# Kernel tuning notes

Measured on AMD Instinct MI355X. Metric: run time of the kernel, lower is better.

## Reference

```python
import jax, jax.numpy as jnp
import numpy as np

TOP_K = 2000
NUM_DETS = 1000
BASE_LAYER_RANGE = (24.0, 48.0, 24.0, 48.0)  # (min_y, max_y, min_x, max_x) from db.configs


def _topk(heat, K):
    # heat: [B, C, H, W] -> topk over flattened C*H*W (CornerNet-style)
    B, C, H, W = heat.shape
    scores, inds = jax.lax.top_k(heat.reshape(B, -1), K)
    clses = inds // (H * W)
    sp_inds = inds % (H * W)            # spatial index into H*W
    ys = (sp_inds // W).astype(heat.dtype)
    xs = (sp_inds % W).astype(heat.dtype)
    return scores, sp_inds, clses, ys, xs


def _transpose_and_gather(feat, ind):
    # feat: [B, C, H, W], ind: [B, K] spatial indices -> [B, K, C]
    B, C, H, W = feat.shape
    feat = feat.transpose(0, 2, 3, 1).reshape(B, H * W, C)
    return feat[jnp.arange(B)[:, None], ind]


def _gather_feat(feat, ind):
    # feat: [B, N, C], ind: [B, K] -> [B, K, C]
    B = feat.shape[0]
    return feat[jnp.arange(B)[:, None], ind]


def _decode_layer(heat, tl_regr, br_regr, H0, W0, layer_idx):
    B, C, H, W = heat.shape
    dt = heat.dtype
    height_scale = 8.0 * H0 / H
    width_scale = 8.0 * W0 / W
    K = min(TOP_K, H * W)
    scores, inds, clses, ys, xs = _topk(heat, K)
    ys = ys.reshape(B, K, 1)
    xs = xs.reshape(B, K, 1)
    tlr = _transpose_and_gather(tl_regr, inds).reshape(B, K, 1, 2)
    brr = _transpose_and_gather(br_regr, inds).reshape(B, K, 1, 2)
    min_y, max_y, min_x, max_x = [v / 8.0 / 2.0 for v in BASE_LAYER_RANGE]
    tl_xs = xs - ((max_x - min_x) * tlr[..., 0] + (max_x + min_x) / 2.0)
    tl_ys = ys - ((max_y - min_y) * tlr[..., 1] + (max_y + min_y) / 2.0)
    br_xs = xs + ((max_x - min_x) * brr[..., 0] + (max_x + min_x) / 2.0)
    br_ys = ys + ((max_y - min_y) * brr[..., 1] + (max_y + min_y) / 2.0)
    bboxes = jnp.stack((tl_xs, tl_ys, br_xs, br_ys), axis=3)  # [B, K, 1, 4]
    sc = scores.reshape(B, K, 1)
    invalid = (br_xs < tl_xs) | (br_ys < tl_ys)
    sc = jnp.where(invalid, jnp.asarray(-1.0, dt), sc)
    sc = sc.reshape(B, -1)
    nd = min(NUM_DETS, sc.shape[1])
    sc, top = jax.lax.top_k(sc, nd)
    sc = sc[:, :, None]
    bboxes = _gather_feat(bboxes.reshape(B, -1, 4), top)
    bboxes = bboxes * jnp.asarray([width_scale, height_scale, width_scale, height_scale], dt)
    # layer_detections: zeros [B, nd, 7]; [:,:,:5] = cat([scores, bboxes]); then row 6 set to i
    det = jnp.concatenate([sc, bboxes, jnp.zeros((B, nd, 2), dt)], axis=2)
    det = det.at[:, 6, :].set(jnp.asarray(float(layer_idx), dt))  # faithful to `[:, 6] = i`
    return det


def setup_inputs() -> dict:
    key = jax.random.key(0)
    ks = jax.random.split(key, 9)
    B, C = 16, 80
    sizes = [(128, 128), (64, 64), (32, 32)]
    inp = {}
    for i, (H, W) in enumerate(sizes):
        inp[f"heat{i}"] = jax.random.uniform(ks[3 * i], (B, C, H, W), dtype=jnp.float32)
        inp[f"tl{i}"] = jax.random.normal(ks[3 * i + 1], (B, 2, H, W), dtype=jnp.float32)
        inp[f"br{i}"] = jax.random.normal(ks[3 * i + 2], (B, 2, H, W), dtype=jnp.float32)
    return inp


def reference(heat0, heat1, heat2, tl0, tl1, tl2, br0, br1, br2):
    heats = [heat0, heat1, heat2]
    tls = [tl0, tl1, tl2]
    brs = [br0, br1, br2]
    _, _, H0, W0 = heats[0].shape
    dets = [_decode_layer(heats[i], tls[i], brs[i], H0, W0, i) for i in range(3)]
    detections = jnp.concatenate(dets, axis=1)  # [B, sum_nd, 7]
    nd = min(NUM_DETS, detections.shape[1])
    _, top = jax.lax.top_k(detections[:, :, 0], nd)
    return _gather_feat(detections, top)
```

## Files before the change

kernel.cpp:

```cpp
#include <hip/hip_runtime.h>


#define NB 1024
#define CAP2 2048
#define CHUNK 32768

__device__ __forceinline__ unsigned int ord_f32(float f) {
    unsigned int b = __float_as_uint(f);
    return (b & 0x80000000u) ? ~b : (b | 0x80000000u);
}
__device__ __forceinline__ float unord_f32(unsigned int o) {
    unsigned int b = (o & 0x80000000u) ? (o & 0x7fffffffu) : ~o;
    return __uint_as_float(b);
}
__device__ __forceinline__ int bucket_of(float f) {
    int bi = (int)(f * (float)NB);
    bi = bi < 0 ? 0 : (bi > NB - 1 ? NB - 1 : bi);
    return bi;
}

__device__ __forceinline__ int layer_N(int l)  { return (l == 0) ? 1310720 : (l == 1) ? 327680 : 81920; }
__device__ __forceinline__ int nchunks(int l)  { return (l == 0) ? 40 : (l == 1) ? 10 : 3; }
__device__ __forceinline__ int hist_base(int l){ return (l == 0) ? 0 : (l == 1) ? 640 : 800; }
__device__ __forceinline__ int TL_of(int l)    { return (l == 0) ? NB - 4 : (l == 1) ? NB - 16 : NB - 32; }
__device__ __forceinline__ int bl_cap(int l)   { return (l == 0) ? 512 : (l == 1) ? 1024 : 2048; }
__device__ __forceinline__ int loose_base(int l){ return (l == 0) ? 0 : (l == 1) ? 327680 : 491520; }

__global__ __launch_bounds__(256) void fused_kernel(
    const float* __restrict__ h0, const float* __restrict__ h1, const float* __restrict__ h2,
    int* __restrict__ ph, int* __restrict__ pbc, unsigned long long* __restrict__ loose)
{
    int l = blockIdx.z, b = blockIdx.y, chunk = blockIdx.x;
    int nc = nchunks(l);
    if (chunk >= nc) return;
    int N = layer_N(l);
    int elems = min(CHUNK, N - chunk * CHUNK);
    const float* heat = (l == 0) ? h0 : (l == 1) ? h1 : h2;
    int TL = TL_of(l);

    __shared__ int lh[NB];
    __shared__ int lc;
    __shared__ unsigned long long lbuf[2048];
    for (int i = threadIdx.x; i < NB; i += 256) lh[i] = 0;
    if (threadIdx.x == 0) lc = 0;
    __syncthreads();

    const float4* p = (const float4*)(heat + (size_t)b * N + (size_t)chunk * CHUNK);
    int base = chunk * CHUNK;
    int n4 = elems >> 2;
    for (int i = threadIdx.x; i < n4; i += 256) {
        float4 v = p[i];
        float vs[4] = {v.x, v.y, v.z, v.w};
#pragma unroll
        for (int cc = 0; cc < 4; cc++) {
            int bk = bucket_of(vs[cc]);
            atomicAdd(&lh[bk], 1);
            if (bk >= TL) {
                int pos = atomicAdd(&lc, 1);
                if (pos < 2048) {
                    unsigned int idx = (unsigned int)(base + 4 * i + cc);
                    lbuf[pos] = ((unsigned long long)ord_f32(vs[cc]) << 32) | (unsigned int)(~idx);
                }
            }
        }
    }
    __syncthreads();
    int pidx = hist_base(l) + b * nc + chunk;
    int* dst = ph + (size_t)pidx * NB;
    for (int i = threadIdx.x; i < NB; i += 256) dst[i] = lh[i];
    if (threadIdx.x == 0) pbc[pidx] = lc;
    int cap = bl_cap(l);
    int n = min(lc, min(cap, 2048));
    unsigned long long* seg = loose + loose_base(l) + (size_t)(b * nc + chunk) * cap;
    for (int i = threadIdx.x; i < n; i += 256) seg[i] = lbuf[i];
}

__global__ __launch_bounds__(256) void partition_kernel(
    const float* __restrict__ h0, const float* __restrict__ h1, const float* __restrict__ h2,
    const int* __restrict__ ph, const int* __restrict__ pbc,
    const unsigned long long* __restrict__ loose,
    int* __restrict__ cnt, unsigned long long* __restrict__ cand)
{
    int b = blockIdx.x & 15;
    int l = blockIdx.x >> 4;
    int bl = l * 16 + b;
    int K = (l == 2) ? 1024 : 2000;
    int nc = nchunks(l);
    int cap = bl_cap(l);
    const int* hbase = ph + (size_t)(hist_base(l) + b * nc) * NB;

    __shared__ int hh[NB];
    __shared__ int seg[256];
    __shared__ int st;
    __shared__ int repf;
    __shared__ int lc[2];
    __shared__ unsigned long long lbuf[2][2048];
    int tid = threadIdx.x;

    int s4 = 0;
    for (int j = 0; j < 4; j++) {
        int bkt = tid * 4 + j;
        int s = 0;
        for (int c = 0; c < nc; c++) s += hbase[(size_t)c * NB + bkt];
        hh[bkt] = s;
        s4 += s;
    }
    seg[tid] = s4;
    if (tid == 0) { repf = 0; lc[0] = 0; lc[1] = 0; }
    __syncthreads();
    if (tid == 0) {
        int acc = 0, si;
        for (si = 255; si >= 0; si--) {
            if (acc + seg[si] >= K) break;
            acc += seg[si];
        }
        if (si < 0) si = 0;
        int bidx = si * 4 + 3;
        for (; bidx > si * 4; bidx--) {
            acc += hh[bidx];
            if (acc >= K) break;
        }
        st = bidx;
        if (bidx < TL_of(l)) repf = 1;
    }
    __syncthreads();
    int t = st;
    for (int c = tid; c < nc; c += 256)
        if (pbc[hist_base(l) + b * nc + c] > min(cap, 2048)) repf = 1;
    __syncthreads();

    if (!repf) {
        const unsigned long long* lb = loose + loose_base(l) + (size_t)b * nc * cap;
        for (int c = 0; c < nc; c++) {
            int n_c = min(pbc[hist_base(l) + b * nc + c], min(cap, 2048));
            const unsigned long long* sg = lb + (size_t)c * cap;
            for (int i = tid; i < n_c; i += 256) {
                unsigned long long key = sg[i];
                int bk = bucket_of(unord_f32((unsigned int)(key >> 32)));
                if (bk >= t) {
                    int which = (bk > t) ? 0 : 1;
                    int pos = atomicAdd(&lc[which], 1);
                    if (pos < 2048) lbuf[which][pos] = key;
                }
            }
        }
    } else {
        int N = layer_N(l);
        const float* heat = (l == 0) ? h0 : (l == 1) ? h1 : h2;
        const float4* p = (const float4*)(heat + (size_t)b * N);
        for (int i = tid; i < (N >> 2); i += 256) {
            float4 v = p[i];
            float vs[4] = {v.x, v.y, v.z, v.w};
#pragma unroll
            for (int cc = 0; cc < 4; cc++) {
                int bk = bucket_of(vs[cc]);
                if (bk >= t) {
                    int which = (bk > t) ? 0 : 1;
                    int pos = atomicAdd(&lc[which], 1);
                    if (pos < 2048) {
                        unsigned int idx = (unsigned int)(4 * i + cc);
                        lbuf[which][pos] = ((unsigned long long)ord_f32(vs[cc]) << 32) | (unsigned int)(~idx);
                    }
                }
            }
        }
    }
    __syncthreads();
#pragma unroll
    for (int w = 0; w < 2; w++) {
        int n = min(lc[w], CAP2);
        if (tid == 0) cnt[bl * 2 + w] = n;
        unsigned long long* cd = cand + ((size_t)bl * 2 + w) * CAP2;
        for (int i = tid; i < n; i += 256) cd[i] = lbuf[w][i];
    }
}


__device__ __forceinline__ unsigned long long shfl_xor_u64(unsigned long long a, int j) {
    unsigned int lo = (unsigned int)a, hi = (unsigned int)(a >> 32);
    lo = (unsigned int)__shfl_xor((int)lo, j, 64);
    hi = (unsigned int)__shfl_xor((int)hi, j, 64);
    return ((unsigned long long)hi << 32) | lo;
}

template<int K, int J>
struct PhaseH {
    static __device__ __forceinline__ void run(unsigned long long (&v)[8], int base, int lane) {
        constexpr int JR = J >> 6;
#pragma unroll
        for (int r = 0; r < 8; r++) {
            if ((r & JR) == 0) {
                int i = base | (r << 6) | lane;
                unsigned long long a = v[r], bb = v[r | JR];
                bool sw = ((i & K) == 0) ? (a < bb) : (a > bb);
                if (sw) { v[r] = bb; v[r | JR] = a; }
            }
        }
        PhaseH<K, (J >> 1)>::run(v, base, lane);
    }
};

template<int K>
struct PhaseH<K, 32> {
    static __device__ __forceinline__ void run(unsigned long long (&v)[8], int base, int lane) {
#pragma unroll
        for (int js = 32; js >= 1; js >>= 1) {
            if (K > js) {
#pragma unroll
                for (int r = 0; r < 8; r++) {
                    unsigned long long a = v[r];
                    unsigned long long w = shfl_xor_u64(a, js);
                    int i = base | (r << 6) | lane;
                    bool upper = (lane & js) != 0;
                    bool keep_max = (((i & K) == 0) != upper);
                    bool agw = a > w;
                    v[r] = (keep_max == agw) ? a : w;
                }
            }
        }
    }
};

template<int K>
struct StageH {
    static __device__ __forceinline__ void run(unsigned long long (&v)[8], int base, int lane) {
        PhaseH<K, (K > 64 ? (K >> 1) : 32)>::run(v, base, lane);
        StageH<(K << 1)>::run(v, base, lane);
    }
};
template<>
struct StageH<1024> {
    static __device__ __forceinline__ void run(unsigned long long (&)[8], int, int) {}
};

template<int K, int J>
__device__ __forceinline__ void lds_exchange(unsigned long long (&v)[8],
                                             unsigned long long* lds, int base, int lane) {
    __syncthreads();
#pragma unroll
    for (int r = 0; r < 8; r++) lds[base | (r << 6) | lane] = v[r];
    __syncthreads();
#pragma unroll
    for (int r = 0; r < 8; r++) {
        int i = base | (r << 6) | lane;
        unsigned long long w = lds[i ^ J];
        bool upper = (i & J) != 0;
        bool keep_max = (((i & K) == 0) != upper);
        bool agw = v[r] > w;
        v[r] = (keep_max == agw) ? v[r] : w;
    }
}

__global__ __launch_bounds__(256) void sort_kernel(const int* __restrict__ cnt,
                                                   unsigned long long* __restrict__ cand)
{
    int idx = blockIdx.x;
    int n = min(cnt[idx], CAP2);
    unsigned long long* src = cand + (size_t)idx * CAP2;
    __shared__ unsigned long long lds[CAP2];
    int tid = threadIdx.x;
    int lane = tid & 63;
    int base = (tid >> 6) << 9;

    unsigned long long v[8];
#pragma unroll
    for (int r = 0; r < 8; r++) {
        int i = base | (r << 6) | lane;
        v[r] = (i < n) ? src[i] : 0ull;
    }

    StageH<2>::run(v, base, lane);

    lds_exchange<1024, 512>(v, lds, base, lane);
    PhaseH<1024, 256>::run(v, base, lane);

    lds_exchange<2048, 1024>(v, lds, base, lane);
    lds_exchange<2048, 512>(v, lds, base, lane);
    PhaseH<2048, 256>::run(v, base, lane);

#pragma unroll
    for (int r = 0; r < 8; r++) src[base | (r << 6) | lane] = v[r];
}

__global__ __launch_bounds__(1024) void build_kernel(
    const float* __restrict__ t0, const float* __restrict__ t1, const float* __restrict__ t2,
    const float* __restrict__ r0, const float* __restrict__ r1, const float* __restrict__ r2,
    const int* __restrict__ cnt, const unsigned long long* __restrict__ cand,
    float* __restrict__ det)
{
    int l = blockIdx.x >> 4;
    int b = blockIdx.x & 15;
    int bl = l * 16 + b;
    int HW = (l == 0) ? 16384 : (l == 1) ? 4096 : 1024;
    int W  = (l == 0) ? 128 : (l == 1) ? 64 : 32;
    int K  = (l == 2) ? 1024 : 2000;
    float scale = (l == 0) ? 8.f : (l == 1) ? 16.f : 32.f;
    const float* tlp = (l == 0) ? t0 : (l == 1) ? t1 : t2;
    const float* brp = (l == 0) ? r0 : (l == 1) ? r1 : r2;

    int n_hi = min(cnt[bl * 2], CAP2);
    const unsigned long long* hi = cand + (size_t)(bl * 2) * CAP2;
    const unsigned long long* bd = cand + (size_t)(bl * 2 + 1) * CAP2;

    __shared__ int wsum[16];
    int tid = threadIdx.x;
    int lane = tid & 63, wid = tid >> 6;

    float s_[2], bx_[2][4];
    int f_[2];
#pragma unroll
    for (int q = 0; q < 2; q++) {
        int k = 2 * tid + q;
        f_[q] = 0;
        if (k < K) {
            unsigned long long kk = (k < n_hi) ? hi[k] : bd[k - n_hi];
            unsigned int idx = ~(unsigned int)kk;
            float score = unord_f32((unsigned int)(kk >> 32));
            int sp = (int)(idx % (unsigned)HW);
            float xs = (float)(sp % W), ys = (float)(sp / W);
            float tv0 = tlp[((size_t)b * 2 + 0) * HW + sp];
            float tv1 = tlp[((size_t)b * 2 + 1) * HW + sp];
            float bv0 = brp[((size_t)b * 2 + 0) * HW + sp];
            float bv1 = brp[((size_t)b * 2 + 1) * HW + sp];
            float tlx = __fsub_rn(xs, __fadd_rn(__fmul_rn(1.5f, tv0), 2.25f));
            float tly = __fsub_rn(ys, __fadd_rn(__fmul_rn(1.5f, tv1), 2.25f));
            float brx = __fadd_rn(xs, __fadd_rn(__fmul_rn(1.5f, bv0), 2.25f));
            float bry = __fadd_rn(ys, __fadd_rn(__fmul_rn(1.5f, bv1), 2.25f));
            bool invalid = (brx < tlx) || (bry < tly);
            f_[q] = invalid ? 0 : 1;
            s_[q] = invalid ? -1.0f : score;
            bx_[q][0] = __fmul_rn(tlx, scale);
            bx_[q][1] = __fmul_rn(tly, scale);
            bx_[q][2] = __fmul_rn(brx, scale);
            bx_[q][3] = __fmul_rn(bry, scale);
        }
    }
    int mysum = f_[0] + f_[1];

    int x = mysum;
#pragma unroll
    for (int off = 1; off < 64; off <<= 1) {
        int y = __shfl_up(x, off, 64);
        if (lane >= off) x += y;
    }
    if (lane == 63) wsum[wid] = x;
    __syncthreads();
    if (wid == 0 && lane < 16) {
        int s = wsum[lane];
#pragma unroll
        for (int off = 1; off < 16; off <<= 1) {
            int y = __shfl_up(s, off, 64);
            if (lane >= off) s += y;
        }
        wsum[lane] = s;
    }
    __syncthreads();
    int wave_off = (wid > 0) ? wsum[wid - 1] : 0;
    int V = wsum[15];
    int base_excl = (x + wave_off) - mysum;

    float* dbase = det + ((size_t)b * 3000 + (size_t)l * 1000) * 7;
#pragma unroll
    for (int q = 0; q < 2; q++) {
        int k = 2 * tid + q;
        if (k < K) {
            int pos = base_excl + (q == 1 ? f_[0] : 0);
            int rank = f_[q] ? pos : V + (k - pos);
            if (rank < 1000 && rank != 6) {
                float* drow = dbase + (size_t)rank * 7;
                drow[0] = s_[q];
                drow[1] = bx_[q][0];
                drow[2] = bx_[q][1];
                drow[3] = bx_[q][2];
                drow[4] = bx_[q][3];
                drow[5] = 0.f;
                drow[6] = 0.f;
            }
        }
    }
    if (tid == 0) {
        float lv = (float)l;
        float* drow = dbase + 6 * 7;
#pragma unroll
        for (int j = 0; j < 7; j++) drow[j] = lv;
    }
}

__device__ __forceinline__ bool key_gt(float sa, int ga, float sb, int gb) {
    return (sa > sb) || (sa == sb && ga < gb);
}

__global__ __launch_bounds__(1024) void final_kernel(const float* __restrict__ det,
                                                     float* __restrict__ out)
{
    int b = blockIdx.x;
    __shared__ float sc[3000];
    int tid = threadIdx.x;
    const float* dbase = det + (size_t)b * 3000 * 7;
    for (int i = tid; i < 3000; i += 1024) sc[i] = dbase[(size_t)i * 7];
    __syncthreads();

    for (int e = tid; e < 3000; e += 1024) {
        float se = sc[e];
        int ge = e;
        int rank = 0;
#pragma unroll
        for (int lp = 0; lp < 3; lp++) {
            int lo = 0, hiB = 999;
            while (lo < hiB) {
                int mid = (lo + hiB) >> 1;
                int p = mid + (mid >= 6 ? 1 : 0);
                int g = lp * 1000 + p;
                if (key_gt(sc[g], g, se, ge)) lo = mid + 1; else hiB = mid;
            }
            rank += lo;
        }
#pragma unroll
        for (int ls = 0; ls < 3; ls++) {
            int g = ls * 1000 + 6;
            if (g != e && key_gt((float)ls, g, se, ge)) rank++;
        }
        if (rank < 1000) {
            const float* src = dbase + (size_t)e * 7;
            float* dst = out + ((size_t)b * 1000 + rank) * 7;
#pragma unroll
            for (int j = 0; j < 7; j++) dst[j] = src[j];
        }
    }
}

extern "C" void kernel_launch(void* const* d_in, const int* in_sizes, int n_in,
                              void* d_out, int out_size, void* d_ws, size_t ws_size,
                              hipStream_t stream)
{
    (void)in_sizes; (void)n_in; (void)out_size; (void)ws_size;
    const float* h0 = (const float*)d_in[0];
    const float* t0 = (const float*)d_in[1];
    const float* r0 = (const float*)d_in[2];
    const float* h1 = (const float*)d_in[3];
    const float* t1 = (const float*)d_in[4];
    const float* r1 = (const float*)d_in[5];
    const float* h2 = (const float*)d_in[6];
    const float* t2 = (const float*)d_in[7];
    const float* r2 = (const float*)d_in[8];
    float* out = (float*)d_out;

    char* ws = (char*)d_ws;
    int* ph   = (int*)ws;
    int* pbc  = (int*)(ws + 3473408);
    unsigned long long* loose = (unsigned long long*)(ws + 3476800);
    int* cnt  = (int*)(ws + 8195392);
    unsigned long long* cand  = (unsigned long long*)(ws + 8195776);
    float* det = (float*)(ws + 9768640);

    fused_kernel<<<dim3(40, 16, 3), 256, 0, stream>>>(h0, h1, h2, ph, pbc, loose);
    partition_kernel<<<48, 256, 0, stream>>>(h0, h1, h2, ph, pbc, loose, cnt, cand);
    sort_kernel<<<96, 256, 0, stream>>>(cnt, cand);
    build_kernel<<<48, 1024, 0, stream>>>(t0, t1, t2, r0, r1, r2, cnt, cand, det);
    final_kernel<<<16, 1024, 0, stream>>>(det, out);
}
```

Baseline: 255.7 us.

## Drop histogram pass; collect over fixed threshold and sort all candidates directly

The collect kernel no longer builds a per-chunk 1024-bucket histogram with shared atomics. It only gathers elements above a fixed per-layer threshold into smaller per-chunk segments. The separate partition kernel is removed, and the sort kernel concatenates the segments into a 4096-entry bitonic sort per batch-layer, holding 16 values per thread. That removes one launch, the histogram atomics and their global writes. In exchange the sort is larger, and a slow fallback (full-layer histogram plus rescan by one block) runs if too few or too many candidates are collected.

```diff
diff --git a/kernel.cpp b/kernel.cpp
--- a/kernel.cpp
+++ b/kernel.cpp
@@ -2,7 +2,6 @@
 
 
 #define NB 1024
-#define CAP2 2048
 #define CHUNK 32768
 
 __device__ __forceinline__ unsigned int ord_f32(float f) {
@@ -19,16 +18,16 @@
     return bi;
 }
 
-__device__ __forceinline__ int layer_N(int l)  { return (l == 0) ? 1310720 : (l == 1) ? 327680 : 81920; }
-__device__ __forceinline__ int nchunks(int l)  { return (l == 0) ? 40 : (l == 1) ? 10 : 3; }
-__device__ __forceinline__ int hist_base(int l){ return (l == 0) ? 0 : (l == 1) ? 640 : 800; }
-__device__ __forceinline__ int TL_of(int l)    { return (l == 0) ? NB - 4 : (l == 1) ? NB - 16 : NB - 32; }
-__device__ __forceinline__ int bl_cap(int l)   { return (l == 0) ? 512 : (l == 1) ? 1024 : 2048; }
-__device__ __forceinline__ int loose_base(int l){ return (l == 0) ? 0 : (l == 1) ? 327680 : 491520; }
-
-__global__ __launch_bounds__(256) void fused_kernel(
+__device__ __forceinline__ int layer_N(int l)   { return (l == 0) ? 1310720 : (l == 1) ? 327680 : 81920; }
+__device__ __forceinline__ int nchunks(int l)   { return (l == 0) ? 40 : (l == 1) ? 10 : 3; }
+__device__ __forceinline__ int chunk_base(int l){ return (l == 0) ? 0 : (l == 1) ? 640 : 800; }
+__device__ __forceinline__ float TL_of(int l)   { return (l == 0) ? 0.998046875f : (l == 1) ? 0.9921875f : 0.98125f; }
+__device__ __forceinline__ int seg_cap(int l)   { return (l == 0) ? 256 : (l == 1) ? 768 : 1024; }
+__device__ __forceinline__ int loose_base(int l){ return (l == 0) ? 0 : (l == 1) ? 163840 : 286720; }
+
+__global__ __launch_bounds__(256) void collect_kernel(
     const float* __restrict__ h0, const float* __restrict__ h1, const float* __restrict__ h2,
-    int* __restrict__ ph, int* __restrict__ pbc, unsigned long long* __restrict__ loose)
+    int* __restrict__ pbc, unsigned long long* __restrict__ loose)
 {
     int l = blockIdx.z, b = blockIdx.y, chunk = blockIdx.x;
     int nc = nchunks(l);
@@ -36,12 +35,10 @@
     int N = layer_N(l);
     int elems = min(CHUNK, N - chunk * CHUNK);
     const float* heat = (l == 0) ? h0 : (l == 1) ? h1 : h2;
-    int TL = TL_of(l);
-
-    __shared__ int lh[NB];
+    float TL = TL_of(l);
+
     __shared__ int lc;
-    __shared__ unsigned long long lbuf[2048];
-    for (int i = threadIdx.x; i < NB; i += 256) lh[i] = 0;
+    __shared__ unsigned long long lbuf[1024];
     if (threadIdx.x == 0) lc = 0;
     __syncthreads();
 
@@ -53,11 +50,9 @@
         float vs[4] = {v.x, v.y, v.z, v.w};
 #pragma unroll
         for (int cc = 0; cc < 4; cc++) {
-            int bk = bucket_of(vs[cc]);
-            atomicAdd(&lh[bk], 1);
-            if (bk >= TL) {
+            if (vs[cc] >= TL) {
                 int pos = atomicAdd(&lc, 1);
-                if (pos < 2048) {
+                if (pos < 1024) {
                     unsigned int idx = (unsigned int)(base + 4 * i + cc);
                     lbuf[pos] = ((unsigned long long)ord_f32(vs[cc]) << 32) | (unsigned int)(~idx);
                 }
@@ -65,114 +60,12 @@
         }
     }
     __syncthreads();
-    int pidx = hist_base(l) + b * nc + chunk;
-    int* dst = ph + (size_t)pidx * NB;
-    for (int i = threadIdx.x; i < NB; i += 256) dst[i] = lh[i];
+    int pidx = chunk_base(l) + b * nc + chunk;
     if (threadIdx.x == 0) pbc[pidx] = lc;
-    int cap = bl_cap(l);
-    int n = min(lc, min(cap, 2048));
+    int cap = seg_cap(l);
+    int n = min(lc, cap);
     unsigned long long* seg = loose + loose_base(l) + (size_t)(b * nc + chunk) * cap;
     for (int i = threadIdx.x; i < n; i += 256) seg[i] = lbuf[i];
-}
-
-__global__ __launch_bounds__(256) void partition_kernel(
-    const float* __restrict__ h0, const float* __restrict__ h1, const float* __restrict__ h2,
-    const int* __restrict__ ph, const int* __restrict__ pbc,
-    const unsigned long long* __restrict__ loose,
-    int* __restrict__ cnt, unsigned long long* __restrict__ cand)
-{
-    int b = blockIdx.x & 15;
-    int l = blockIdx.x >> 4;
-    int bl = l * 16 + b;
-    int K = (l == 2) ? 1024 : 2000;
-    int nc = nchunks(l);
-    int cap = bl_cap(l);
-    const int* hbase = ph + (size_t)(hist_base(l) + b * nc) * NB;
-
-    __shared__ int hh[NB];
-    __shared__ int seg[256];
-    __shared__ int st;
-    __shared__ int repf;
-    __shared__ int lc[2];
-    __shared__ unsigned long long lbuf[2][2048];
-    int tid = threadIdx.x;
-
-    int s4 = 0;
-    for (int j = 0; j < 4; j++) {
-        int bkt = tid * 4 + j;
-        int s = 0;
-        for (int c = 0; c < nc; c++) s += hbase[(size_t)c * NB + bkt];
-        hh[bkt] = s;
-        s4 += s;
-    }
-    seg[tid] = s4;
-    if (tid == 0) { repf = 0; lc[0] = 0; lc[1] = 0; }
-    __syncthreads();
-    if (tid == 0) {
-        int acc = 0, si;
-        for (si = 255; si >= 0; si--) {
-            if (acc + seg[si] >= K) break;
-            acc += seg[si];
-        }
-        if (si < 0) si = 0;
-        int bidx = si * 4 + 3;
-        for (; bidx > si * 4; bidx--) {
-            acc += hh[bidx];
-            if (acc >= K) break;
-        }
-        st = bidx;
-        if (bidx < TL_of(l)) repf = 1;
-    }
-    __syncthreads();
-    int t = st;
-    for (int c = tid; c < nc; c += 256)
-        if (pbc[hist_base(l) + b * nc + c] > min(cap, 2048)) repf = 1;
-    __syncthreads();
-
-    if (!repf) {
-        const unsigned long long* lb = loose + loose_base(l) + (size_t)b * nc * cap;
-        for (int c = 0; c < nc; c++) {
-            int n_c = min(pbc[hist_base(l) + b * nc + c], min(cap, 2048));
-            const unsigned long long* sg = lb + (size_t)c * cap;
-            for (int i = tid; i < n_c; i += 256) {
-                unsigned long long key = sg[i];
-                int bk = bucket_of(unord_f32((unsigned int)(key >> 32)));
-                if (bk >= t) {
-                    int which = (bk > t) ? 0 : 1;
-                    int pos = atomicAdd(&lc[which], 1);
-                    if (pos < 2048) lbuf[which][pos] = key;
-                }
-            }
-        }
-    } else {
-        int N = layer_N(l);
-        const float* heat = (l == 0) ? h0 : (l == 1) ? h1 : h2;
-        const float4* p = (const float4*)(heat + (size_t)b * N);
-        for (int i = tid; i < (N >> 2); i += 256) {
-            float4 v = p[i];
-            float vs[4] = {v.x, v.y, v.z, v.w};
-#pragma unroll
-            for (int cc = 0; cc < 4; cc++) {
-                int bk = bucket_of(vs[cc]);
-                if (bk >= t) {
-                    int which = (bk > t) ? 0 : 1;
-                    int pos = atomicAdd(&lc[which], 1);
-                    if (pos < 2048) {
-                        unsigned int idx = (unsigned int)(4 * i + cc);
-                        lbuf[which][pos] = ((unsigned long long)ord_f32(vs[cc]) << 32) | (unsigned int)(~idx);
-                    }
-                }
-            }
-        }
-    }
-    __syncthreads();
-#pragma unroll
-    for (int w = 0; w < 2; w++) {
-        int n = min(lc[w], CAP2);
-        if (tid == 0) cnt[bl * 2 + w] = n;
-        unsigned long long* cd = cand + ((size_t)bl * 2 + w) * CAP2;
-        for (int i = tid; i < n; i += 256) cd[i] = lbuf[w][i];
-    }
 }
 
 
@@ -184,11 +77,11 @@
 }
 
 template<int K, int J>
-struct PhaseH {
-    static __device__ __forceinline__ void run(unsigned long long (&v)[8], int base, int lane) {
+struct P16 {
+    static __device__ __forceinline__ void run(unsigned long long (&v)[16], int base, int lane) {
         constexpr int JR = J >> 6;
 #pragma unroll
-        for (int r = 0; r < 8; r++) {
+        for (int r = 0; r < 16; r++) {
             if ((r & JR) == 0) {
                 int i = base | (r << 6) | lane;
                 unsigned long long a = v[r], bb = v[r | JR];
@@ -196,18 +89,18 @@
                 if (sw) { v[r] = bb; v[r | JR] = a; }
             }
         }
-        PhaseH<K, (J >> 1)>::run(v, base, lane);
+        P16<K, (J >> 1)>::run(v, base, lane);
     }
 };
 
 template<int K>
-struct PhaseH<K, 32> {
-    static __device__ __forceinline__ void run(unsigned long long (&v)[8], int base, int lane) {
+struct P16<K, 32> {
+    static __device__ __forceinline__ void run(unsigned long long (&v)[16], int base, int lane) {
 #pragma unroll
         for (int js = 32; js >= 1; js >>= 1) {
             if (K > js) {
 #pragma unroll
-                for (int r = 0; r < 8; r++) {
+                for (int r = 0; r < 16; r++) {
                     unsigned long long a = v[r];
                     unsigned long long w = shfl_xor_u64(a, js);
                     int i = base | (r << 6) | lane;
@@ -222,26 +115,26 @@
 };
 
 template<int K>
-struct StageH {
-    static __device__ __forceinline__ void run(unsigned long long (&v)[8], int base, int lane) {
-        PhaseH<K, (K > 64 ? (K >> 1) : 32)>::run(v, base, lane);
-        StageH<(K << 1)>::run(v, base, lane);
+struct S16 {
+    static __device__ __forceinline__ void run(unsigned long long (&v)[16], int base, int lane) {
+        P16<K, (K > 64 ? (K >> 1) : 32)>::run(v, base, lane);
+        S16<(K << 1)>::run(v, base, lane);
     }
 };
 template<>
-struct StageH<1024> {
-    static __device__ __forceinline__ void run(unsigned long long (&)[8], int, int) {}
+struct S16<2048> {
+    static __device__ __forceinline__ void run(unsigned long long (&)[16], int, int) {}
 };
 
 template<int K, int J>
-__device__ __forceinline__ void lds_exchange(unsigned long long (&v)[8],
-                                             unsigned long long* lds, int base, int lane) {
-    __syncthreads();
-#pragma unroll
-    for (int r = 0; r < 8; r++) lds[base | (r << 6) | lane] = v[r];
-    __syncthreads();
-#pragma unroll
-    for (int r = 0; r < 8; r++) {
+__device__ __forceinline__ void lds_exchange16(unsigned long long (&v)[16],
+                                               unsigned long long* lds, int base, int lane) {
+    __syncthreads();
+#pragma unroll
+    for (int r = 0; r < 16; r++) lds[base | (r << 6) | lane] = v[r];
+    __syncthreads();
+#pragma unroll
+    for (int r = 0; r < 16; r++) {
         int i = base | (r << 6) | lane;
         unsigned long long w = lds[i ^ J];
         bool upper = (i & J) != 0;
@@ -251,42 +144,103 @@
     }
 }
 
-__global__ __launch_bounds__(256) void sort_kernel(const int* __restrict__ cnt,
-                                                   unsigned long long* __restrict__ cand)
+__global__ __launch_bounds__(256) void sort_kernel(
+    const float* __restrict__ h0, const float* __restrict__ h1, const float* __restrict__ h2,
+    const int* __restrict__ pbc, const unsigned long long* __restrict__ loose,
+    unsigned long long* __restrict__ cand)
 {
-    int idx = blockIdx.x;
-    int n = min(cnt[idx], CAP2);
-    unsigned long long* src = cand + (size_t)idx * CAP2;
-    __shared__ unsigned long long lds[CAP2];
+    int bl = blockIdx.x;
+    int l = bl >> 4, b = bl & 15;
+    int K = (l == 2) ? 1024 : 2000;
+    int nc = nchunks(l);
+    int cap = seg_cap(l);
     int tid = threadIdx.x;
     int lane = tid & 63;
-    int base = (tid >> 6) << 9;
-
-    unsigned long long v[8];
-#pragma unroll
-    for (int r = 0; r < 8; r++) {
-        int i = base | (r << 6) | lane;
-        v[r] = (i < n) ? src[i] : 0ull;
-    }
-
-    StageH<2>::run(v, base, lane);
-
-    lds_exchange<1024, 512>(v, lds, base, lane);
-    PhaseH<1024, 256>::run(v, base, lane);
-
-    lds_exchange<2048, 1024>(v, lds, base, lane);
-    lds_exchange<2048, 512>(v, lds, base, lane);
-    PhaseH<2048, 256>::run(v, base, lane);
-
-#pragma unroll
-    for (int r = 0; r < 8; r++) src[base | (r << 6) | lane] = v[r];
+    int base = (tid >> 6) << 10;
+
+    __shared__ unsigned long long lds[4096];
+    __shared__ int offs[41];
+    __shared__ int s_bad, s_tot;
+
+    if (tid == 0) {
+        int o = 0, bad = 0;
+        const int* pb = pbc + chunk_base(l) + b * nc;
+        for (int c = 0; c < nc; c++) {
+            int raw = pb[c];
+            if (raw > cap) bad = 1;
+            offs[c] = o;
+            o += min(raw, cap);
+        }
+        offs[nc] = o;
+        if (o < K || o > 4096) bad = 1;
+        s_bad = bad;
+        s_tot = o;
+    }
+    __syncthreads();
+
+    if (!s_bad) {
+        const unsigned long long* lb = loose + loose_base(l) + (size_t)b * nc * cap;
+        for (int c = 0; c < nc; c++) {
+            int o = offs[c], n_c = offs[c + 1] - o;
+            const unsigned long long* sg = lb + (size_t)c * cap;
+            for (int i = tid; i < n_c; i += 256) lds[o + i] = sg[i];
+        }
+        for (int i = s_tot + tid; i < 4096; i += 256) lds[i] = 0ull;
+    } else {
+        __shared__ int lh[NB];
+        __shared__ int st, lc2;
+        for (int i = tid; i < NB; i += 256) lh[i] = 0;
+        if (tid == 0) lc2 = 0;
+        __syncthreads();
+        int N = layer_N(l);
+        const float* hp = ((l == 0) ? h0 : (l == 1) ? h1 : h2) + (size_t)b * N;
+        for (int i = tid; i < N; i += 256) atomicAdd(&lh[bucket_of(hp[i])], 1);
+        __syncthreads();
+        if (tid == 0) {
+            int acc = 0, bidx;
+            for (bidx = NB - 1; bidx > 0; bidx--) {
+                acc += lh[bidx];
+                if (acc >= K) break;
+            }
+            st = bidx;
+        }
+        __syncthreads();
+        int t = st;
+        for (int i = tid; i < N; i += 256) {
+            float x = hp[i];
+            if (bucket_of(x) >= t) {
+                int pos = atomicAdd(&lc2, 1);
+                if (pos < 4096)
+                    lds[pos] = ((unsigned long long)ord_f32(x) << 32) | (unsigned int)(~(unsigned int)i);
+            }
+        }
+        __syncthreads();
+        for (int i = min(lc2, 4096) + tid; i < 4096; i += 256) lds[i] = 0ull;
+    }
+    __syncthreads();
+
+    unsigned long long v[16];
+#pragma unroll
+    for (int r = 0; r < 16; r++) v[r] = lds[base | (r << 6) | lane];
+
+    S16<2>::run(v, base, lane);
+
+    lds_exchange16<2048, 1024>(v, lds, base, lane);
+    P16<2048, 512>::run(v, base, lane);
+
+    lds_exchange16<4096, 2048>(v, lds, base, lane);
+    lds_exchange16<4096, 1024>(v, lds, base, lane);
+    P16<4096, 512>::run(v, base, lane);
+
+    unsigned long long* cd = cand + (size_t)bl * 4096;
+#pragma unroll
+    for (int r = 0; r < 16; r++) cd[base | (r << 6) | lane] = v[r];
 }
 
 __global__ __launch_bounds__(1024) void build_kernel(
     const float* __restrict__ t0, const float* __restrict__ t1, const float* __restrict__ t2,
     const float* __restrict__ r0, const float* __restrict__ r1, const float* __restrict__ r2,
-    const int* __restrict__ cnt, const unsigned long long* __restrict__ cand,
-    float* __restrict__ det)
+    const unsigned long long* __restrict__ cand, float* __restrict__ det)
 {
     int l = blockIdx.x >> 4;
     int b = blockIdx.x & 15;
@@ -298,9 +252,7 @@
     const float* tlp = (l == 0) ? t0 : (l == 1) ? t1 : t2;
     const float* brp = (l == 0) ? r0 : (l == 1) ? r1 : r2;
 
-    int n_hi = min(cnt[bl * 2], CAP2);
-    const unsigned long long* hi = cand + (size_t)(bl * 2) * CAP2;
-    const unsigned long long* bd = cand + (size_t)(bl * 2 + 1) * CAP2;
+    const unsigned long long* srt = cand + (size_t)bl * 4096;
 
     __shared__ int wsum[16];
     int tid = threadIdx.x;
@@ -313,7 +265,7 @@
         int k = 2 * tid + q;
         f_[q] = 0;
         if (k < K) {
-            unsigned long long kk = (k < n_hi) ? hi[k] : bd[k - n_hi];
+            unsigned long long kk = srt[k];
             unsigned int idx = ~(unsigned int)kk;
             float score = unord_f32((unsigned int)(kk >> 32));
             int sp = (int)(idx % (unsigned)HW);
@@ -446,16 +398,13 @@
     float* out = (float*)d_out;
 
     char* ws = (char*)d_ws;
-    int* ph   = (int*)ws;
-    int* pbc  = (int*)(ws + 3473408);
-    unsigned long long* loose = (unsigned long long*)(ws + 3476800);
-    int* cnt  = (int*)(ws + 8195392);
-    unsigned long long* cand  = (unsigned long long*)(ws + 8195776);
-    float* det = (float*)(ws + 9768640);
-
-    fused_kernel<<<dim3(40, 16, 3), 256, 0, stream>>>(h0, h1, h2, ph, pbc, loose);
-    partition_kernel<<<48, 256, 0, stream>>>(h0, h1, h2, ph, pbc, loose, cnt, cand);
-    sort_kernel<<<96, 256, 0, stream>>>(cnt, cand);
-    build_kernel<<<48, 1024, 0, stream>>>(t0, t1, t2, r0, r1, r2, cnt, cand, det);
+    int* pbc  = (int*)ws;
+    unsigned long long* loose = (unsigned long long*)(ws + 3392);
+    unsigned long long* cand  = (unsigned long long*)(ws + 2690368);
+    float* det = (float*)(ws + 4263232);
+
+    collect_kernel<<<dim3(40, 16, 3), 256, 0, stream>>>(h0, h1, h2, pbc, loose);
+    sort_kernel<<<48, 256, 0, stream>>>(h0, h1, h2, pbc, loose, cand);
+    build_kernel<<<48, 1024, 0, stream>>>(t0, t1, t2, r0, r1, r2, cand, det);
     final_kernel<<<16, 1024, 0, stream>>>(det, out);
 }
```

After: 249.6 us. 1.02x faster.
